# Kernel tuning notes

Measured on AMD Instinct MI355X. Metric: run time of the kernel, lower is better.

## Reference

```python
import jax, jax.numpy as jnp
import numpy as np
import math

B = 2048
INPUT_SIZE = 1024
OUTPUT_SIZE = 512
SPONGE = 1024
ACT = 256
REC = 256
STORE = ACT + REC  # 512
DEPTH = 8
BDEPTH = 10
NEUTRAL_C = 1.0
SQRT2 = math.sqrt(2.0)


def _make_structure():
    # Deterministic stand-in for the module's random.sample-based recall wiring.
    rng = np.random.RandomState(0)
    half = (SPONGE + 1) // 2
    shuffle_perm = np.array([i // 2 + (i % 2) * half for i in range(SPONGE)], dtype=np.int64)
    unused = []
    recall = []
    for i in range(DEPTH):
        unused.extend(range(i * STORE, (i + 1) * STORE))
        sel = rng.choice(len(unused), size=REC, replace=False)
        sel_set = set(sel.tolist())
        recall.append([unused[k] for k in sorted(sel_set)])
        unused = [u for k, u in enumerate(unused) if k not in sel_set]
    out_mem = np.array(sorted(unused), dtype=np.int64)  # 2048 leftover memory columns
    bf_size = len(out_mem) + SPONGE  # 3072
    bf_depth = int(math.ceil(math.log2(bf_size)))  # 12
    bf_half = (bf_size + 1) // 2
    bf_perm = np.array([i // 2 + (i % 2) * bf_half for i in range(bf_size)], dtype=np.int64)
    return shuffle_perm, np.array(recall, dtype=np.int64), out_mem, bf_perm, bf_size, bf_depth


def setup_inputs() -> dict:
    key = jax.random.key(0)
    ks = jax.random.split(key, 6)
    shuffle_perm, recall_idx, out_mem_idx, bf_perm, bf_size, bf_depth = _make_structure()
    return {
        "X": jax.random.normal(ks[0], (B, INPUT_SIZE), jnp.float32),
        "scales": jnp.ones((INPUT_SIZE,), jnp.float32),
        "angles": jax.random.uniform(ks[1], (DEPTH, BDEPTH, SPONGE // 2), jnp.float32) * (2 * math.pi),
        "act_bias": jax.random.normal(ks[2], (DEPTH, ACT), jnp.float32),
        "act_activation": jax.random.normal(ks[3], (DEPTH, ACT), jnp.float32),
        "act_curvature": jax.random.normal(ks[4], (DEPTH, ACT), jnp.float32),
        "bf_angles": jax.random.uniform(ks[5], (bf_depth, bf_size // 2), jnp.float32) * (2 * math.pi),
        "shuffle_perm": jnp.asarray(shuffle_perm),
        "recall_idx": jnp.asarray(recall_idx),
        "output_mem_idx": jnp.asarray(out_mem_idx),
        "bf_perm": jnp.asarray(bf_perm),
    }


def _base_activation(x, c):
    # In the source, `a` is overwritten with torch.tensor(1.0), so a == 1.
    t = (math.pi / 4) / c
    y0 = (1.0 / c) * (1.0 / SQRT2 - math.cos(math.pi / 2))  # = 1/(c*sqrt(2))
    m0 = math.sin(math.pi / 2)  # = 1
    y1 = (1.0 / c) * (1.0 / SQRT2 - 1.0)
    m1 = math.sin(0.0)  # = 0
    mid = (1.0 / c) * (1.0 / SQRT2 - jnp.cos(math.pi / 4 + c * x))
    return jnp.where(x > t, y0 + m0 * (x - t), jnp.where(x < -t, y1 + m1 * (x + t), mid))


def _butterfly(x, angles, perm):
    # angles: [n_layers, exch]; shuffle -> Givens rotation per pair, extra passthrough
    exch = angles.shape[1]
    for j in range(angles.shape[0]):
        s = x[:, perm]
        x1, x2 = s[:, :exch], s[:, exch:2 * exch]
        ca, sa = jnp.cos(angles[j]), jnp.sin(angles[j])
        x = jnp.concatenate([ca * x1 + sa * x2, -sa * x1 + ca * x2, s[:, 2 * exch:]], axis=1)
    return x


def reference(X, scales, angles, act_bias, act_activation, act_curvature, bf_angles,
              shuffle_perm, recall_idx, output_mem_idx, bf_perm):
    Xs = X * scales
    sponge = Xs[:, :SPONGE]  # input_size == sponge_size: no zero pad, memory[0] is empty
    mem = jnp.zeros((Xs.shape[0], DEPTH * STORE), Xs.dtype)
    for i in range(DEPTH):
        sponge = _butterfly(sponge, angles[i], shuffle_perm)
        x1 = sponge[:, STORE:STORE + ACT] + act_bias[i]  # activation_position == store_size
        c = 0.5 * NEUTRAL_C * (act_curvature[i] + jnp.sqrt(act_curvature[i] ** 2 + 1.0))
        ap = _base_activation(x1, c)
        am = _base_activation(-x1, c)
        act_out = jnp.stack([ap, am], axis=2).reshape(ap.shape[0], 2 * ACT)  # interleave +/-
        mem = mem.at[:, i * STORE:(i + 1) * STORE].set(sponge[:, :STORE])
        recall = mem[:, recall_idx[i]]  # indices only address already-filled columns
        # [act_out | sponge[store:act_pos] (empty) | sponge[act_pos+ACT:] | recall]
        sponge = jnp.concatenate([act_out, sponge[:, STORE + ACT:], recall], axis=1)
    pre = jnp.concatenate([mem[:, output_mem_idx], sponge], axis=1)  # [B, 3072]
    out = _butterfly(pre, bf_angles, bf_perm)
    return out[:, :OUTPUT_SIZE]
```

## Files before the change

### kernel.cpp

```cpp
#include <hip/hip_runtime.h>
#include <math.h>

#define NB 2048
#define DEPTH 8

#define FTAB_OFF    0
#define BF01_OFF    81920
#define BFF_OFF     88064
#define ACT4_OFF    98304
#define PHYS_OFF    106496
#define PHYSR_OFF   110592
#define PHYSO2_OFF  112640

__global__ void tab_precompute(const float* __restrict__ angles,
                               const float* __restrict__ bf_angles,
                               const float* __restrict__ act_bias,
                               const float* __restrict__ act_curv,
                               float* __restrict__ ws) {
    int id = blockIdx.x * 256 + threadIdx.x;
    if (id < 40960) {
        int w  = id & 3;
        int t  = (id >> 2) & 255;
        int dg = id >> 10;
        int d = dg / 5, g = dg - 5 * d;
        int a = 2 * (t & 127) + (t >> 7);
        int pair = (w == 0) ? a : (w == 1) ? (a + 256)
                 : (w == 2) ? (2 * a) : (2 * a + 1);
        int st = 2 * g + (w >> 1);
        float ang = angles[(d * 10 + st) * 512 + pair];
        float s, c; sincosf(ang, &s, &c);
        ws[FTAB_OFF + 2 * id]     = c;
        ws[FTAB_OFF + 2 * id + 1] = s;
    } else if (id < 44032) {
        int e = id - 40960;
        int w = e & 3; int ti = e >> 2;
        int t = ti / 3; int i = ti - 3 * t;
        int a = t + 256 * i;
        int pair = (w == 0) ? a : (w == 1) ? (a + 768)
                 : (w == 2) ? (2 * a) : (2 * a + 1);
        int stage = (w < 2) ? 0 : 1;
        float ang = bf_angles[stage * 1536 + pair];
        float s, c; sincosf(ang, &s, &c);
        ws[BF01_OFF + 2 * e]     = c;
        ws[BF01_OFF + 2 * e + 1] = s;
    } else if (id < 49152) {
        int e = id - 44032;
        int f = e >> 10; int rem = e & 1023; int t = rem >> 2; int w = rem & 3;
        int P;
        if (f == 0) P = 3 * t;
        else { int k = 8 - 2 * f; P = ((t >> (2 * f)) * (768 >> k)) + (t & ((256 >> k) - 1)); }
        int pair = (w == 0) ? P : (w == 1) ? (P + 768)
                 : (w == 2) ? (2 * P) : (2 * P + 1);
        int stage = (w < 2) ? (2 + 2 * f) : (3 + 2 * f);
        float ang = bf_angles[stage * 1536 + pair];
        float s, c; sincosf(ang, &s, &c);
        ws[BFF_OFF + 2 * e]     = c;
        ws[BFF_OFF + 2 * e + 1] = s;
    } else if (id < 51200) {
        int ida = id - 49152;
        float cu = act_curv[ida];
        float c  = 0.5f * (cu + sqrtf(cu * cu + 1.0f));
        ((float4*)(ws + ACT4_OFF))[ida] =
            make_float4(act_bias[ida], c, 1.0f / c, 0.0f);
    }
}

__global__ void phys_precompute(const int* __restrict__ recall_idx,
                                const int* __restrict__ out_mem_idx,
                                float* __restrict__ ws) {
    __shared__ int physL[4096];
    int t = threadIdx.x;
    for (int q = 0; q < 4; ++q) {
        int v = t + q * 1024;
        int p;
        for (;;) {
            int d = v >> 9, j = v & 511;
            if (d == 0)  { p = j; break; }
            if (j < 256) { p = 256 + d * 256 + j; break; }
            v = recall_idx[(d - 1) * 256 + (j - 256)];
        }
        physL[t + q * 1024] = p;
        ((int*)(ws + PHYS_OFF))[t + q * 1024] = p;
    }
    __syncthreads();
    for (int q = 0; q < 2; ++q) {
        int i = t + q * 1024;
        ((int*)(ws + PHYSR_OFF))[i] = physL[recall_idx[i]];
    }
    for (int e = t; e < 3072; e += 1024) {
        int tt = e / 12; int r = e - 12 * tt; int i = r >> 2; int k = r & 3;
        int a = tt + 256 * i;
        int tl = a >> 1, th = a & 1;
        int pos = tl + 1536 * th + 384 * k;
        int val = (pos < 2048) ? physL[out_mem_idx[pos]] : (2304 + (pos - 2048));
        ((int*)(ws + PHYSO2_OFF))[e] = val;
    }
}

__device__ __forceinline__ float actf(float x, float c, float ic) {
    const float is2 = 0.70710678118654752f;
    float tt = 0.78539816339744831f * ic;
    float y0 = is2 * ic;
    float y1 = (is2 - 1.0f) * ic;
    float mid = ic * (is2 - __cosf(0.78539816339744831f + c * x));
    return x > tt ? (y0 + (x - tt)) : (x < -tt ? y1 : mid);
}

__device__ __forceinline__ int swz(int p) {
    return (p & 1) | ((p & 0x3C) >> 1) | ((((p >> 6) ^ (p >> 1)) & 1) << 5)
         | (((p >> 1) & 1) << 6) | (p & 0x380);
}

__launch_bounds__(256, 8)
__global__ void sponge_kernel(const float* __restrict__ X,
                              const float* __restrict__ scales,
                              const float* __restrict__ ws,
                              float* __restrict__ out) {
    __shared__ float lds[4352];
    float* memb = lds;
    float* pb0  = lds + 2304;
    float* pb1  = lds + 3328;
    const int t   = threadIdx.x;
    const int row = blockIdx.x;

    const float4* bf01  = (const float4*)(ws + BF01_OFF);
    const float4* bff   = (const float4*)(ws + BFF_OFF);
    const float4* act4  = (const float4*)(ws + ACT4_OFF);
    const int* phys   = (const int*)(ws + PHYS_OFF);
    const int* physr  = (const int*)(ws + PHYSR_OFF);
    const int* physo2 = (const int*)(ws + PHYSO2_OFF);

    const int tl = t & 127, th = t >> 7;
    const int b  = tl + th * 512;
    const int a  = 2 * tl + th;

    const int wA0 = swz(2 * a), wA1 = swz(2 * a + 512);
    const int rd0 = swz(b), rd1 = swz(b + 128), rd2 = swz(b + 256), rd3 = swz(b + 384);
    const int zmem = swz(2 * t);
    const int u = t - 128;
    int za0 = 0, za1 = 0, za2 = 0, za3 = 0, zk0 = 0, zk1 = 0;
    if (t < 128) {
        int k0 = t >> 1;
        za0 = swz(512 + k0);       za1 = swz(512 + k0 + 64);
        za2 = swz(512 + k0 + 128); za3 = swz(512 + k0 + 192);
    } else {
        zk0 = swz(768 + u); zk1 = swz(896 + u);
    }

    float h0, h1, h2, h3;
    {
        const float* Xr = X + (size_t)row * 1024;
        h0 = Xr[b]       * scales[b];
        h1 = Xr[b + 128] * scales[b + 128];
        h2 = Xr[b + 256] * scales[b + 256];
        h3 = Xr[b + 384] * scales[b + 384];
    }

    float* wbuf = pb0;
    float* rbuf = pb1;
    const float4* ft = (const float4*)(ws + FTAB_OFF) + 2 * t;

    for (int d = 0; d < DEPTH; ++d) {
        for (int g = 0; g < 5; ++g) {
            float4 csA = ft[0], csB = ft[1]; ft += 512;
            float g0 =  csA.x * h0 + csA.y * h2;
            float g2 = -csA.y * h0 + csA.x * h2;
            float g1 =  csA.z * h1 + csA.w * h3;
            float g3 = -csA.w * h1 + csA.z * h3;
            float f0 =  csB.x * g0 + csB.y * g1;
            float f2 = -csB.y * g0 + csB.x * g1;
            float f1 =  csB.z * g2 + csB.w * g3;
            float f3 = -csB.w * g2 + csB.z * g3;
            *(float2*)(wbuf + wA0) = make_float2(f0, f1);
            *(float2*)(wbuf + wA1) = make_float2(f2, f3);
            { float* tmp = wbuf; wbuf = rbuf; rbuf = tmp; }
            __syncthreads();
            if (g < 4) {
                h0 = rbuf[rd0]; h1 = rbuf[rd1]; h2 = rbuf[rd2]; h3 = rbuf[rd3];
            }
        }
        const float* z = rbuf;
        float2 mv = *(const float2*)(z + zmem);
        int2 pm = ((const int2*)(phys + d * 512))[t];
        memb[pm.x] = mv.x;
        memb[pm.y] = mv.y;
        int r0 = 0, r1 = 0;
        if (t < 128) {
            float x10 = z[za0], x11 = z[za1], x12 = z[za2], x13 = z[za3];
            int k0 = t >> 1;
            float4 a0 = act4[d * 256 + k0];
            float4 a1 = act4[d * 256 + k0 + 64];
            float4 a2 = act4[d * 256 + k0 + 128];
            float4 a3 = act4[d * 256 + k0 + 192];
            float sgn = (t & 1) ? -1.0f : 1.0f;
            h0 = actf(sgn * (x10 + a0.x), a0.y, a0.z);
            h1 = actf(sgn * (x11 + a1.x), a1.y, a1.z);
            h2 = actf(sgn * (x12 + a2.x), a2.y, a2.z);
            h3 = actf(sgn * (x13 + a3.x), a3.y, a3.z);
        } else {
            h0 = z[zk0];
            h1 = z[zk1];
            r0 = physr[d * 256 + u];
            r1 = physr[d * 256 + u + 128];
        }
        __syncthreads();
        if (t >= 128) {
            h2 = memb[r0];
            h3 = memb[r1];
        }
    }

    lds[2304 + b]       = h0;
    lds[2304 + b + 128] = h1;
    lds[2304 + b + 256] = h2;
    lds[2304 + b + 384] = h3;
    __syncthreads();
    int4 pg0 = ((const int4*)(physo2 + t * 12))[0];
    int4 pg1 = ((const int4*)(physo2 + t * 12))[1];
    int4 pg2 = ((const int4*)(physo2 + t * 12))[2];
    float v[12];
    v[0] = lds[pg0.x]; v[1]  = lds[pg0.y]; v[2]  = lds[pg0.z]; v[3]  = lds[pg0.w];
    v[4] = lds[pg1.x]; v[5]  = lds[pg1.y]; v[6]  = lds[pg1.z]; v[7]  = lds[pg1.w];
    v[8] = lds[pg2.x]; v[9]  = lds[pg2.y]; v[10] = lds[pg2.z]; v[11] = lds[pg2.w];
    __syncthreads();
    float* buf = lds;
#pragma unroll
    for (int i = 0; i < 3; ++i) {
        float4 c01 = bf01[(t * 3 + i) * 2];
        float4 c23 = bf01[(t * 3 + i) * 2 + 1];
        float q0 = v[4 * i], q1 = v[4 * i + 1], q2 = v[4 * i + 2], q3 = v[4 * i + 3];
        float g0 =  c01.x * q0 + c01.y * q2;
        float g2 = -c01.y * q0 + c01.x * q2;
        float g1 =  c01.z * q1 + c01.w * q3;
        float g3 = -c01.w * q1 + c01.z * q3;
        float y0 =  c23.x * g0 + c23.y * g1;
        float y2 = -c23.y * g0 + c23.x * g1;
        float y1 =  c23.z * g2 + c23.w * g3;
        float y3 = -c23.w * g2 + c23.z * g3;
        *(float2*)(buf + 2 * t + 512 * i)        = make_float2(y0, y1);
        *(float2*)(buf + 2 * t + 512 * i + 1536) = make_float2(y2, y3);
    }
    __syncthreads();

#pragma unroll
    for (int f = 0; f < 4; ++f) {
        int P;
        if (f == 0) P = 3 * t;
        else { const int k = 8 - 2 * f;
               P = ((t >> (2 * f)) * (768 >> k)) + (t & ((256 >> k) - 1)); }
        int base = (P >> 1) + (P & 1) * 1536;
        float4 csS = bff[(f * 256 + t) * 2];
        float4 csT = bff[(f * 256 + t) * 2 + 1];
        float x1p = buf[base], x1q = buf[base + 384];
        float x2p = buf[base + 768], x2q = buf[base + 1152];
        float o1P =  csS.x * x1p + csS.y * x2p;
        float o2P = -csS.y * x1p + csS.x * x2p;
        float o1Q =  csS.z * x1q + csS.w * x2q;
        float o2Q = -csS.w * x1q + csS.z * x2q;
        float y0 =  csT.x * o1P + csT.y * o1Q;
        float y2 = -csT.y * o1P + csT.x * o1Q;
        float y1 =  csT.z * o2P + csT.w * o2Q;
        float y3 = -csT.w * o2P + csT.z * o2Q;
        __syncthreads();
        *(float2*)(buf + 2 * P)        = make_float2(y0, y1);
        *(float2*)(buf + 2 * P + 1536) = make_float2(y2, y3);
        __syncthreads();
    }

    {
        int base = (t >> 1) + (t & 1) * 1536;
        float4 csS = bff[(4 * 256 + t) * 2];
        float4 csT = bff[(4 * 256 + t) * 2 + 1];
        float x1p = buf[base], x1q = buf[base + 384];
        float x2p = buf[base + 768], x2q = buf[base + 1152];
        float o1P =  csS.x * x1p + csS.y * x2p;
        float o2P = -csS.y * x1p + csS.x * x2p;
        float o1Q =  csS.z * x1q + csS.w * x2q;
        float o2Q = -csS.w * x1q + csS.z * x2q;
        float y0 = csT.x * o1P + csT.y * o1Q;
        float y1 = csT.z * o2P + csT.w * o2Q;
        *(float2*)(out + (size_t)row * 512 + 2 * t) = make_float2(y0, y1);
    }
}

extern "C" void kernel_launch(void* const* d_in, const int* in_sizes, int n_in,
                              void* d_out, int out_size, void* d_ws, size_t ws_size,
                              hipStream_t stream) {
    const float* X          = (const float*)d_in[0];
    const float* scales     = (const float*)d_in[1];
    const float* angles     = (const float*)d_in[2];
    const float* act_bias   = (const float*)d_in[3];
    const float* act_curv   = (const float*)d_in[5];
    const float* bf_angles  = (const float*)d_in[6];
    const int*   recall_idx  = (const int*)d_in[8];
    const int*   out_mem_idx = (const int*)d_in[9];

    float* ws = (float*)d_ws;

    tab_precompute<<<200, 256, 0, stream>>>(angles, bf_angles, act_bias, act_curv, ws);
    phys_precompute<<<1, 1024, 0, stream>>>(recall_idx, out_mem_idx, ws);
    sponge_kernel<<<NB, 256, 0, stream>>>(X, scales, ws, (float*)d_out);
}
```

Baseline: 135.6 us.

## Process two batch rows per block to share twiddle loads and barriers

Each block now handles two rows at once with separate LDS regions, so every twiddle-table load and every __syncthreads is shared by two rows. The grid is halved and launch bounds drop to 4 blocks per SM to allow the extra registers. The aim is to cut global table traffic and sync overhead per row and raise ILP. The cost is more registers and LDS per block, fewer resident blocks, and fewer total blocks (1024) to fill the CUs.

```diff
diff --git a/kernel.cpp b/kernel.cpp
--- a/kernel.cpp
+++ b/kernel.cpp
@@ -111,17 +111,16 @@
          | (((p >> 1) & 1) << 6) | (p & 0x380);
 }
 
-__launch_bounds__(256, 8)
+__launch_bounds__(256, 4)
 __global__ void sponge_kernel(const float* __restrict__ X,
                               const float* __restrict__ scales,
                               const float* __restrict__ ws,
                               float* __restrict__ out) {
-    __shared__ float lds[4352];
-    float* memb = lds;
-    float* pb0  = lds + 2304;
-    float* pb1  = lds + 3328;
-    const int t   = threadIdx.x;
-    const int row = blockIdx.x;
+    __shared__ float lds[8704];
+    float* L0 = lds;
+    float* L1 = lds + 4352;
+    const int t = threadIdx.x;
+    const int rowA = blockIdx.x * 2;
 
     const float4* bf01  = (const float4*)(ws + BF01_OFF);
     const float4* bff   = (const float4*)(ws + BFF_OFF);
@@ -147,99 +146,138 @@
         zk0 = swz(768 + u); zk1 = swz(896 + u);
     }
 
-    float h0, h1, h2, h3;
+    float hA0, hA1, hA2, hA3, hB0, hB1, hB2, hB3;
     {
-        const float* Xr = X + (size_t)row * 1024;
-        h0 = Xr[b]       * scales[b];
-        h1 = Xr[b + 128] * scales[b + 128];
-        h2 = Xr[b + 256] * scales[b + 256];
-        h3 = Xr[b + 384] * scales[b + 384];
-    }
-
-    float* wbuf = pb0;
-    float* rbuf = pb1;
+        const float* Xr0 = X + (size_t)rowA * 1024;
+        const float* Xr1 = Xr0 + 1024;
+        float s0 = scales[b], s1 = scales[b + 128], s2 = scales[b + 256], s3 = scales[b + 384];
+        hA0 = Xr0[b] * s0; hA1 = Xr0[b + 128] * s1;
+        hA2 = Xr0[b + 256] * s2; hA3 = Xr0[b + 384] * s3;
+        hB0 = Xr1[b] * s0; hB1 = Xr1[b + 128] * s1;
+        hB2 = Xr1[b + 256] * s2; hB3 = Xr1[b + 384] * s3;
+    }
+
+    int woff = 2304, roff = 3328;
     const float4* ft = (const float4*)(ws + FTAB_OFF) + 2 * t;
 
     for (int d = 0; d < DEPTH; ++d) {
         for (int g = 0; g < 5; ++g) {
             float4 csA = ft[0], csB = ft[1]; ft += 512;
-            float g0 =  csA.x * h0 + csA.y * h2;
-            float g2 = -csA.y * h0 + csA.x * h2;
-            float g1 =  csA.z * h1 + csA.w * h3;
-            float g3 = -csA.w * h1 + csA.z * h3;
-            float f0 =  csB.x * g0 + csB.y * g1;
-            float f2 = -csB.y * g0 + csB.x * g1;
-            float f1 =  csB.z * g2 + csB.w * g3;
-            float f3 = -csB.w * g2 + csB.z * g3;
-            *(float2*)(wbuf + wA0) = make_float2(f0, f1);
-            *(float2*)(wbuf + wA1) = make_float2(f2, f3);
-            { float* tmp = wbuf; wbuf = rbuf; rbuf = tmp; }
+            float g0 =  csA.x * hA0 + csA.y * hA2;
+            float g2 = -csA.y * hA0 + csA.x * hA2;
+            float g1 =  csA.z * hA1 + csA.w * hA3;
+            float g3 = -csA.w * hA1 + csA.z * hA3;
+            float fA0 =  csB.x * g0 + csB.y * g1;
+            float fA2 = -csB.y * g0 + csB.x * g1;
+            float fA1 =  csB.z * g2 + csB.w * g3;
+            float fA3 = -csB.w * g2 + csB.z * g3;
+            float G0 =  csA.x * hB0 + csA.y * hB2;
+            float G2 = -csA.y * hB0 + csA.x * hB2;
+            float G1 =  csA.z * hB1 + csA.w * hB3;
+            float G3 = -csA.w * hB1 + csA.z * hB3;
+            float fB0 =  csB.x * G0 + csB.y * G1;
+            float fB2 = -csB.y * G0 + csB.x * G1;
+            float fB1 =  csB.z * G2 + csB.w * G3;
+            float fB3 = -csB.w * G2 + csB.z * G3;
+            *(float2*)(L0 + woff + wA0) = make_float2(fA0, fA1);
+            *(float2*)(L0 + woff + wA1) = make_float2(fA2, fA3);
+            *(float2*)(L1 + woff + wA0) = make_float2(fB0, fB1);
+            *(float2*)(L1 + woff + wA1) = make_float2(fB2, fB3);
+            { int tmp = woff; woff = roff; roff = tmp; }
             __syncthreads();
             if (g < 4) {
-                h0 = rbuf[rd0]; h1 = rbuf[rd1]; h2 = rbuf[rd2]; h3 = rbuf[rd3];
+                hA0 = L0[roff + rd0]; hA1 = L0[roff + rd1];
+                hA2 = L0[roff + rd2]; hA3 = L0[roff + rd3];
+                hB0 = L1[roff + rd0]; hB1 = L1[roff + rd1];
+                hB2 = L1[roff + rd2]; hB3 = L1[roff + rd3];
             }
         }
-        const float* z = rbuf;
-        float2 mv = *(const float2*)(z + zmem);
+        const float* z0 = L0 + roff;
+        const float* z1 = L1 + roff;
+        float2 mvA = *(const float2*)(z0 + zmem);
+        float2 mvB = *(const float2*)(z1 + zmem);
         int2 pm = ((const int2*)(phys + d * 512))[t];
-        memb[pm.x] = mv.x;
-        memb[pm.y] = mv.y;
+        L0[pm.x] = mvA.x; L0[pm.y] = mvA.y;
+        L1[pm.x] = mvB.x; L1[pm.y] = mvB.y;
         int r0 = 0, r1 = 0;
         if (t < 128) {
-            float x10 = z[za0], x11 = z[za1], x12 = z[za2], x13 = z[za3];
             int k0 = t >> 1;
             float4 a0 = act4[d * 256 + k0];
             float4 a1 = act4[d * 256 + k0 + 64];
             float4 a2 = act4[d * 256 + k0 + 128];
             float4 a3 = act4[d * 256 + k0 + 192];
             float sgn = (t & 1) ? -1.0f : 1.0f;
-            h0 = actf(sgn * (x10 + a0.x), a0.y, a0.z);
-            h1 = actf(sgn * (x11 + a1.x), a1.y, a1.z);
-            h2 = actf(sgn * (x12 + a2.x), a2.y, a2.z);
-            h3 = actf(sgn * (x13 + a3.x), a3.y, a3.z);
+            hA0 = actf(sgn * (z0[za0] + a0.x), a0.y, a0.z);
+            hA1 = actf(sgn * (z0[za1] + a1.x), a1.y, a1.z);
+            hA2 = actf(sgn * (z0[za2] + a2.x), a2.y, a2.z);
+            hA3 = actf(sgn * (z0[za3] + a3.x), a3.y, a3.z);
+            hB0 = actf(sgn * (z1[za0] + a0.x), a0.y, a0.z);
+            hB1 = actf(sgn * (z1[za1] + a1.x), a1.y, a1.z);
+            hB2 = actf(sgn * (z1[za2] + a2.x), a2.y, a2.z);
+            hB3 = actf(sgn * (z1[za3] + a3.x), a3.y, a3.z);
         } else {
-            h0 = z[zk0];
-            h1 = z[zk1];
+            hA0 = z0[zk0]; hA1 = z0[zk1];
+            hB0 = z1[zk0]; hB1 = z1[zk1];
             r0 = physr[d * 256 + u];
             r1 = physr[d * 256 + u + 128];
         }
         __syncthreads();
         if (t >= 128) {
-            h2 = memb[r0];
-            h3 = memb[r1];
+            hA2 = L0[r0]; hA3 = L0[r1];
+            hB2 = L1[r0]; hB3 = L1[r1];
         }
     }
 
-    lds[2304 + b]       = h0;
-    lds[2304 + b + 128] = h1;
-    lds[2304 + b + 256] = h2;
-    lds[2304 + b + 384] = h3;
+    L0[2304 + b] = hA0; L0[2304 + b + 128] = hA1;
+    L0[2304 + b + 256] = hA2; L0[2304 + b + 384] = hA3;
+    L1[2304 + b] = hB0; L1[2304 + b + 128] = hB1;
+    L1[2304 + b + 256] = hB2; L1[2304 + b + 384] = hB3;
     __syncthreads();
-    int4 pg0 = ((const int4*)(physo2 + t * 12))[0];
-    int4 pg1 = ((const int4*)(physo2 + t * 12))[1];
-    int4 pg2 = ((const int4*)(physo2 + t * 12))[2];
-    float v[12];
-    v[0] = lds[pg0.x]; v[1]  = lds[pg0.y]; v[2]  = lds[pg0.z]; v[3]  = lds[pg0.w];
-    v[4] = lds[pg1.x]; v[5]  = lds[pg1.y]; v[6]  = lds[pg1.z]; v[7]  = lds[pg1.w];
-    v[8] = lds[pg2.x]; v[9]  = lds[pg2.y]; v[10] = lds[pg2.z]; v[11] = lds[pg2.w];
+
+    float vA0, vA1, vA2, vA3, vA4, vA5, vA6, vA7, vA8, vA9, vA10, vA11;
+    float vB0, vB1, vB2, vB3, vB4, vB5, vB6, vB7, vB8, vB9, vB10, vB11;
+    {
+        int4 pg = ((const int4*)(physo2 + t * 12))[0];
+        vA0 = L0[pg.x]; vA1 = L0[pg.y]; vA2 = L0[pg.z]; vA3 = L0[pg.w];
+        vB0 = L1[pg.x]; vB1 = L1[pg.y]; vB2 = L1[pg.z]; vB3 = L1[pg.w];
+        pg = ((const int4*)(physo2 + t * 12))[1];
+        vA4 = L0[pg.x]; vA5 = L0[pg.y]; vA6 = L0[pg.z]; vA7 = L0[pg.w];
+        vB4 = L1[pg.x]; vB5 = L1[pg.y]; vB6 = L1[pg.z]; vB7 = L1[pg.w];
+        pg = ((const int4*)(physo2 + t * 12))[2];
+        vA8 = L0[pg.x]; vA9 = L0[pg.y]; vA10 = L0[pg.z]; vA11 = L0[pg.w];
+        vB8 = L1[pg.x]; vB9 = L1[pg.y]; vB10 = L1[pg.z]; vB11 = L1[pg.w];
+    }
     __syncthreads();
-    float* buf = lds;
-#pragma unroll
-    for (int i = 0; i < 3; ++i) {
-        float4 c01 = bf01[(t * 3 + i) * 2];
-        float4 c23 = bf01[(t * 3 + i) * 2 + 1];
-        float q0 = v[4 * i], q1 = v[4 * i + 1], q2 = v[4 * i + 2], q3 = v[4 * i + 3];
-        float g0 =  c01.x * q0 + c01.y * q2;
-        float g2 = -c01.y * q0 + c01.x * q2;
-        float g1 =  c01.z * q1 + c01.w * q3;
-        float g3 = -c01.w * q1 + c01.z * q3;
-        float y0 =  c23.x * g0 + c23.y * g1;
-        float y2 = -c23.y * g0 + c23.x * g1;
-        float y1 =  c23.z * g2 + c23.w * g3;
-        float y3 = -c23.w * g2 + c23.z * g3;
-        *(float2*)(buf + 2 * t + 512 * i)        = make_float2(y0, y1);
-        *(float2*)(buf + 2 * t + 512 * i + 1536) = make_float2(y2, y3);
-    }
+
+#define BF01_STEP(i, qA0, qA1, qA2, qA3, qB0, qB1, qB2, qB3)                        \
+    {                                                                               \
+        float4 c01 = bf01[(t * 3 + (i)) * 2];                                       \
+        float4 c23 = bf01[(t * 3 + (i)) * 2 + 1];                                   \
+        float g0 =  c01.x * qA0 + c01.y * qA2;                                      \
+        float g2 = -c01.y * qA0 + c01.x * qA2;                                      \
+        float g1 =  c01.z * qA1 + c01.w * qA3;                                      \
+        float g3 = -c01.w * qA1 + c01.z * qA3;                                      \
+        float y0 =  c23.x * g0 + c23.y * g1;                                        \
+        float y2 = -c23.y * g0 + c23.x * g1;                                        \
+        float y1 =  c23.z * g2 + c23.w * g3;                                        \
+        float y3 = -c23.w * g2 + c23.z * g3;                                        \
+        *(float2*)(L0 + 2 * t + 512 * (i))        = make_float2(y0, y1);            \
+        *(float2*)(L0 + 2 * t + 512 * (i) + 1536) = make_float2(y2, y3);            \
+        g0 =  c01.x * qB0 + c01.y * qB2;                                            \
+        g2 = -c01.y * qB0 + c01.x * qB2;                                            \
+        g1 =  c01.z * qB1 + c01.w * qB3;                                            \
+        g3 = -c01.w * qB1 + c01.z * qB3;                                            \
+        y0 =  c23.x * g0 + c23.y * g1;                                              \
+        y2 = -c23.y * g0 + c23.x * g1;                                              \
+        y1 =  c23.z * g2 + c23.w * g3;                                              \
+        y3 = -c23.w * g2 + c23.z * g3;                                              \
+        *(float2*)(L1 + 2 * t + 512 * (i))        = make_float2(y0, y1);            \
+        *(float2*)(L1 + 2 * t + 512 * (i) + 1536) = make_float2(y2, y3);            \
+    }
+    BF01_STEP(0, vA0, vA1, vA2, vA3, vB0, vB1, vB2, vB3)
+    BF01_STEP(1, vA4, vA5, vA6, vA7, vB4, vB5, vB6, vB7)
+    BF01_STEP(2, vA8, vA9, vA10, vA11, vB8, vB9, vB10, vB11)
+#undef BF01_STEP
     __syncthreads();
 
 #pragma unroll
@@ -251,35 +289,54 @@
         int base = (P >> 1) + (P & 1) * 1536;
         float4 csS = bff[(f * 256 + t) * 2];
         float4 csT = bff[(f * 256 + t) * 2 + 1];
-        float x1p = buf[base], x1q = buf[base + 384];
-        float x2p = buf[base + 768], x2q = buf[base + 1152];
+        float xA1p = L0[base], xA1q = L0[base + 384];
+        float xA2p = L0[base + 768], xA2q = L0[base + 1152];
+        float xB1p = L1[base], xB1q = L1[base + 384];
+        float xB2p = L1[base + 768], xB2q = L1[base + 1152];
+        float o1P =  csS.x * xA1p + csS.y * xA2p;
+        float o2P = -csS.y * xA1p + csS.x * xA2p;
+        float o1Q =  csS.z * xA1q + csS.w * xA2q;
+        float o2Q = -csS.w * xA1q + csS.z * xA2q;
+        float yA0 =  csT.x * o1P + csT.y * o1Q;
+        float yA2 = -csT.y * o1P + csT.x * o1Q;
+        float yA1 =  csT.z * o2P + csT.w * o2Q;
+        float yA3 = -csT.w * o2P + csT.z * o2Q;
+        o1P =  csS.x * xB1p + csS.y * xB2p;
+        o2P = -csS.y * xB1p + csS.x * xB2p;
+        o1Q =  csS.z * xB1q + csS.w * xB2q;
+        o2Q = -csS.w * xB1q + csS.z * xB2q;
+        float yB0 =  csT.x * o1P + csT.y * o1Q;
+        float yB2 = -csT.y * o1P + csT.x * o1Q;
+        float yB1 =  csT.z * o2P + csT.w * o2Q;
+        float yB3 = -csT.w * o2P + csT.z * o2Q;
+        __syncthreads();
+        *(float2*)(L0 + 2 * P)        = make_float2(yA0, yA1);
+        *(float2*)(L0 + 2 * P + 1536) = make_float2(yA2, yA3);
+        *(float2*)(L1 + 2 * P)        = make_float2(yB0, yB1);
+        *(float2*)(L1 + 2 * P + 1536) = make_float2(yB2, yB3);
+        __syncthreads();
+    }
+
+    {
+        int base = (t >> 1) + (t & 1) * 1536;
+        float4 csS = bff[(4 * 256 + t) * 2];
+        float4 csT = bff[(4 * 256 + t) * 2 + 1];
+        float x1p = L0[base], x1q = L0[base + 384];
+        float x2p = L0[base + 768], x2q = L0[base + 1152];
         float o1P =  csS.x * x1p + csS.y * x2p;
         float o2P = -csS.y * x1p + csS.x * x2p;
         float o1Q =  csS.z * x1q + csS.w * x2q;
         float o2Q = -csS.w * x1q + csS.z * x2q;
-        float y0 =  csT.x * o1P + csT.y * o1Q;
-        float y2 = -csT.y * o1P + csT.x * o1Q;
-        float y1 =  csT.z * o2P + csT.w * o2Q;
-        float y3 = -csT.w * o2P + csT.z * o2Q;
-        __syncthreads();
-        *(float2*)(buf + 2 * P)        = make_float2(y0, y1);
-        *(float2*)(buf + 2 * P + 1536) = make_float2(y2, y3);
-        __syncthreads();
-    }
-
-    {
-        int base = (t >> 1) + (t & 1) * 1536;
-        float4 csS = bff[(4 * 256 + t) * 2];
-        float4 csT = bff[(4 * 256 + t) * 2 + 1];
-        float x1p = buf[base], x1q = buf[base + 384];
-        float x2p = buf[base + 768], x2q = buf[base + 1152];
-        float o1P =  csS.x * x1p + csS.y * x2p;
-        float o2P = -csS.y * x1p + csS.x * x2p;
-        float o1Q =  csS.z * x1q + csS.w * x2q;
-        float o2Q = -csS.w * x1q + csS.z * x2q;
-        float y0 = csT.x * o1P + csT.y * o1Q;
-        float y1 = csT.z * o2P + csT.w * o2Q;
-        *(float2*)(out + (size_t)row * 512 + 2 * t) = make_float2(y0, y1);
+        *(float2*)(out + (size_t)rowA * 512 + 2 * t) =
+            make_float2(csT.x * o1P + csT.y * o1Q, csT.z * o2P + csT.w * o2Q);
+        x1p = L1[base]; x1q = L1[base + 384];
+        x2p = L1[base + 768]; x2q = L1[base + 1152];
+        o1P =  csS.x * x1p + csS.y * x2p;
+        o2P = -csS.y * x1p + csS.x * x2p;
+        o1Q =  csS.z * x1q + csS.w * x2q;
+        o2Q = -csS.w * x1q + csS.z * x2q;
+        *(float2*)(out + (size_t)(rowA + 1) * 512 + 2 * t) =
+            make_float2(csT.x * o1P + csT.y * o1Q, csT.z * o2P + csT.w * o2Q);
     }
 }
 
@@ -299,5 +356,5 @@
 
     tab_precompute<<<200, 256, 0, stream>>>(angles, bf_angles, act_bias, act_curv, ws);
     phys_precompute<<<1, 1024, 0, stream>>>(recall_idx, out_mem_idx, ws);
-    sponge_kernel<<<NB, 256, 0, stream>>>(X, scales, ws, (float*)d_out);
-}
+    sponge_kernel<<<NB / 2, 256, 0, stream>>>(X, scales, ws, (float*)d_out);
+}
```

New measurement: 122.3 us. 9.8% less time.
